# Performance work log

Measured on AMD Instinct MI355X. Metric: run time of the kernel, lower is better.

Reference implementation:

```python
import jax, jax.numpy as jnp
import numpy as np

N_NODES = 100000
N_EDGES = 1_600_000
D_IN = 64
DIM_H = 64


def _film_conv(x, src, dst, W_lin, W_film, b_film, W_skip, W_film_skip):
    """PyG FiLMConv, num_relations=1, aggr='mean', act=ReLU.
    lins/lin_skip have no bias; film has bias; film_skip has no bias."""
    n = x.shape[0]
    # skip/self term: (beta_s, gamma_s) = film_skip(x)
    beta_s, gamma_s = jnp.split(x @ W_film_skip, 2, axis=-1)
    out = jax.nn.relu(gamma_s * (x @ W_skip) + beta_s)
    # relation term: FiLM params from target node i, transform source node j
    beta, gamma = jnp.split(x @ W_film + b_film, 2, axis=-1)  # [N, H] each
    h = x @ W_lin                                             # [N, H]
    msg = jax.nn.relu(gamma[dst] * h[src] + beta[dst])        # [E, H] gather+FiLM
    agg = jax.ops.segment_sum(msg, dst, num_segments=n)       # scatter-sum
    deg = jax.ops.segment_sum(jnp.ones((src.shape[0],), msg.dtype), dst,
                              num_segments=n)
    return out + agg / jnp.maximum(deg, 1.0)[:, None]         # mean aggregation


def setup_inputs() -> dict:
    key = jax.random.key(0)
    ks = jax.random.split(key, 12)
    x = jax.random.normal(ks[0], (N_NODES, D_IN), dtype=jnp.float32)
    edge_index = jax.random.randint(ks[1], (2, N_EDGES), 0, N_NODES, dtype=jnp.int64)
    s_in = 1.0 / np.sqrt(D_IN)
    s_h = 1.0 / np.sqrt(DIM_H)
    params = {
        # layer 1 (D_IN -> DIM_H)
        "W_lin1": jax.random.normal(ks[2], (D_IN, DIM_H), jnp.float32) * s_in,
        "W_film1": jax.random.normal(ks[3], (D_IN, 2 * DIM_H), jnp.float32) * s_in,
        "b_film1": jnp.zeros((2 * DIM_H,), jnp.float32),
        "W_skip1": jax.random.normal(ks[4], (D_IN, DIM_H), jnp.float32) * s_in,
        "W_film_skip1": jax.random.normal(ks[5], (D_IN, 2 * DIM_H), jnp.float32) * s_in,
        # layer 2 (DIM_H -> DIM_H)
        "W_lin2": jax.random.normal(ks[6], (DIM_H, DIM_H), jnp.float32) * s_h,
        "W_film2": jax.random.normal(ks[7], (DIM_H, 2 * DIM_H), jnp.float32) * s_h,
        "b_film2": jnp.zeros((2 * DIM_H,), jnp.float32),
        "W_skip2": jax.random.normal(ks[8], (DIM_H, DIM_H), jnp.float32) * s_h,
        "W_film_skip2": jax.random.normal(ks[9], (DIM_H, 2 * DIM_H), jnp.float32) * s_h,
        # final head
        "W_out": jax.random.normal(ks[10], (DIM_H, 1), jnp.float32) * s_h,
        "b_out": jnp.zeros((1,), jnp.float32),
    }
    return {"x": x, "edge_index": edge_index, **params}


def reference(x, edge_index,
              W_lin1, W_film1, b_film1, W_skip1, W_film_skip1,
              W_lin2, W_film2, b_film2, W_skip2, W_film_skip2,
              W_out, b_out):
    src, dst = edge_index[0], edge_index[1]
    h = _film_conv(x, src, dst, W_lin1, W_film1, b_film1, W_skip1, W_film_skip1)
    h = jax.nn.leaky_relu(h, negative_slope=0.01)
    h = _film_conv(h, src, dst, W_lin2, W_film2, b_film2, W_skip2, W_film_skip2)
    h = jax.nn.leaky_relu(h, negative_slope=0.01)
    return h @ W_out + b_out  # [N, 1]
```

## Files before the change

### kernel.cpp

```cpp
#include <hip/hip_runtime.h>
#include <cstddef>


#define THREADS 256
#define NB 256
#define NPSHIFT 9
#define NPSZ 512

typedef unsigned short u16;
typedef unsigned char u8;
typedef unsigned int u32;
typedef short bf16x8 __attribute__((ext_vector_type(8)));
typedef float f32x4 __attribute__((ext_vector_type(4)));
typedef float f32x2 __attribute__((ext_vector_type(2)));

__device__ __forceinline__ u16 f2b(float f) {
  u32 u = __float_as_uint(f);
  u32 r = (u + 0x7FFFu + ((u >> 16) & 1u)) >> 16;
  return (u16)r;
}
__device__ __forceinline__ float b2f(u16 u) {
  return __uint_as_float(((u32)u) << 16);
}
__device__ __forceinline__ u8 f2fp8(float v) {
  return (u8)(__builtin_amdgcn_cvt_pk_fp8_f32(v, v, 0, false) & 0xFF);
}

struct WSrc {
  const float* p;
  int ld;
  int off;
};
struct WPack {
  WSrc m[12];
};

__global__ __launch_bounds__(THREADS) void prep_and_hist(
    WPack wp, u16* __restrict__ Wp, const int* __restrict__ dst,
    int* __restrict__ counts, int E, int CH, int P) {
  int b = blockIdx.x, t = threadIdx.x;
  if (b < 12) {
    WSrc ws = wp.m[b];
    u16* dstp = Wp + b * 4096;
#pragma unroll
    for (int i = 0; i < 16; ++i) {
      int e = t + 256 * i;
      int n = e >> 6, k = e & 63;
      float v = ws.p[(size_t)k * ws.ld + ws.off + n];
      dstp[e ^ ((n & 7) << 3)] = f2b(v);
    }
    return;
  }
  __shared__ int h[256];
  int hb = b - 12;
  h[t] = 0;
  __syncthreads();
  int lo = hb * CH;
  int hi = min(lo + CH, E);
  for (int i = lo + t; i < hi; i += THREADS) atomicAdd(&h[dst[i] >> NPSHIFT], 1);
  __syncthreads();
  if (t < P) counts[t * NB + hb] = h[t];
}

template <int INBF16>
__global__ __launch_bounds__(THREADS) void gemm_mfma(
    const void* __restrict__ Xv, int N, const u16* __restrict__ WpL,
    const float* __restrict__ bfilm, u8* __restrict__ H8, u16* __restrict__ BETA,
    u16* __restrict__ GAMMA, u16* __restrict__ S) {
  __shared__ u16 XT[64 * 64];
  __shared__ u16 WT[6 * 64 * 64];
  int t = threadIdx.x;
  int row0 = blockIdx.x * 64;

  {
    int row = t >> 2, kq = (t & 3) * 16;
    int gr = row0 + row;
    uint4 w0 = {0, 0, 0, 0}, w1 = {0, 0, 0, 0};
    if (gr < N) {
      if (INBF16) {
        const uint4* xp = (const uint4*)((const u16*)Xv + (size_t)gr * 64 + kq);
        w0 = xp[0];
        w1 = xp[1];
      } else {
        const float* xp = (const float*)Xv + (size_t)gr * 64 + kq;
        float4 f0 = ((const float4*)xp)[0];
        float4 f1 = ((const float4*)xp)[1];
        float4 f2 = ((const float4*)xp)[2];
        float4 f3 = ((const float4*)xp)[3];
        w0.x = f2b(f0.x) | ((u32)f2b(f0.y) << 16);
        w0.y = f2b(f0.z) | ((u32)f2b(f0.w) << 16);
        w0.z = f2b(f1.x) | ((u32)f2b(f1.y) << 16);
        w0.w = f2b(f1.z) | ((u32)f2b(f1.w) << 16);
        w1.x = f2b(f2.x) | ((u32)f2b(f2.y) << 16);
        w1.y = f2b(f2.z) | ((u32)f2b(f2.w) << 16);
        w1.z = f2b(f3.x) | ((u32)f2b(f3.y) << 16);
        w1.w = f2b(f3.z) | ((u32)f2b(f3.w) << 16);
      }
    }
    int e = row * 64 + kq;
    int s = (row & 7) << 3;
    *(uint4*)&XT[e ^ s] = w0;
    *(uint4*)&XT[(e + 8) ^ s] = w1;
  }
  {
    const uint4* wsrc = (const uint4*)WpL;
    uint4* wdst = (uint4*)WT;
    for (int i = t; i < 3072; i += THREADS) wdst[i] = wsrc[i];
  }
  __syncthreads();

  int lane = t & 63, wid = t >> 6;
  int arow = wid * 16 + (lane & 15);
  int kb = (lane >> 4) << 3;
  int as = (arow & 7) << 3;
  bf16x8 A0 = *(const bf16x8*)&XT[(arow * 64 + kb) ^ as];
  bf16x8 A1 = *(const bf16x8*)&XT[(arow * 64 + 32 + kb) ^ as];

  auto bfrag = [&](int mat, int ct, int kk) -> bf16x8 {
    int n = ct * 16 + (lane & 15);
    int e = (n * 64 + kk * 32 + kb) ^ ((n & 7) << 3);
    return *(const bf16x8*)&WT[mat * 4096 + e];
  };

  const f32x4 z = {0.f, 0.f, 0.f, 0.f};
  int rbase = wid * 16 + ((lane >> 4) << 2);
  int cbase = lane & 15;

  {
    f32x4 a0[4], a1[4], a2[4];
#pragma unroll
    for (int ct = 0; ct < 4; ++ct) {
      a0[ct] = z;
      a1[ct] = z;
      a2[ct] = z;
    }
#pragma unroll
    for (int ct = 0; ct < 4; ++ct) {
      a0[ct] = __builtin_amdgcn_mfma_f32_16x16x32_bf16(A0, bfrag(0, ct, 0), a0[ct], 0, 0, 0);
      a0[ct] = __builtin_amdgcn_mfma_f32_16x16x32_bf16(A1, bfrag(0, ct, 1), a0[ct], 0, 0, 0);
      a1[ct] = __builtin_amdgcn_mfma_f32_16x16x32_bf16(A0, bfrag(1, ct, 0), a1[ct], 0, 0, 0);
      a1[ct] = __builtin_amdgcn_mfma_f32_16x16x32_bf16(A1, bfrag(1, ct, 1), a1[ct], 0, 0, 0);
      a2[ct] = __builtin_amdgcn_mfma_f32_16x16x32_bf16(A0, bfrag(2, ct, 0), a2[ct], 0, 0, 0);
      a2[ct] = __builtin_amdgcn_mfma_f32_16x16x32_bf16(A1, bfrag(2, ct, 1), a2[ct], 0, 0, 0);
    }
#pragma unroll
    for (int ct = 0; ct < 4; ++ct) {
      int c = ct * 16 + cbase;
#pragma unroll
      for (int r = 0; r < 4; ++r) {
        int gr = row0 + rbase + r;
        if (gr < N) {
          float v = fmaxf(fmaf(a2[ct][r], a0[ct][r], a1[ct][r]), 0.f);
          S[(size_t)gr * 64 + c] = f2b(v);
        }
      }
    }
  }

  {
    f32x4 a0[4], a1[4], a2[4];
#pragma unroll
    for (int ct = 0; ct < 4; ++ct) {
      a0[ct] = z;
      a1[ct] = z;
      a2[ct] = z;
    }
#pragma unroll
    for (int ct = 0; ct < 4; ++ct) {
      a0[ct] = __builtin_amdgcn_mfma_f32_16x16x32_bf16(A0, bfrag(3, ct, 0), a0[ct], 0, 0, 0);
      a0[ct] = __builtin_amdgcn_mfma_f32_16x16x32_bf16(A1, bfrag(3, ct, 1), a0[ct], 0, 0, 0);
      a1[ct] = __builtin_amdgcn_mfma_f32_16x16x32_bf16(A0, bfrag(4, ct, 0), a1[ct], 0, 0, 0);
      a1[ct] = __builtin_amdgcn_mfma_f32_16x16x32_bf16(A1, bfrag(4, ct, 1), a1[ct], 0, 0, 0);
      a2[ct] = __builtin_amdgcn_mfma_f32_16x16x32_bf16(A0, bfrag(5, ct, 0), a2[ct], 0, 0, 0);
      a2[ct] = __builtin_amdgcn_mfma_f32_16x16x32_bf16(A1, bfrag(5, ct, 1), a2[ct], 0, 0, 0);
    }
#pragma unroll
    for (int ct = 0; ct < 4; ++ct) {
      int c = ct * 16 + cbase;
      float bb = bfilm[c];
      float bg = bfilm[64 + c];
#pragma unroll
      for (int r = 0; r < 4; ++r) {
        int gr = row0 + rbase + r;
        if (gr < N) {
          size_t o = (size_t)gr * 64 + c;
          H8[o] = f2fp8(a0[ct][r]);
          BETA[o] = f2b(a1[ct][r] + bb);
          GAMMA[o] = f2b(a2[ct][r] + bg);
        }
      }
    }
  }
}

__global__ __launch_bounds__(THREADS) void scan_block(int* __restrict__ arr,
                                                      int* __restrict__ bsums, int M) {
  __shared__ int ts[THREADS];
  int t = threadIdx.x;
  int base = blockIdx.x * 1024 + t * 4;
  int v0 = 0, v1 = 0, v2 = 0, v3 = 0;
  if (base + 0 < M) v0 = arr[base + 0];
  if (base + 1 < M) v1 = arr[base + 1];
  if (base + 2 < M) v2 = arr[base + 2];
  if (base + 3 < M) v3 = arr[base + 3];
  int s = v0 + v1 + v2 + v3;
  ts[t] = s;
  __syncthreads();
  for (int off = 1; off < THREADS; off <<= 1) {
    int x = (t >= off) ? ts[t - off] : 0;
    __syncthreads();
    ts[t] += x;
    __syncthreads();
  }
  int eb = ts[t] - s;
  if (base + 0 < M) arr[base + 0] = eb;
  if (base + 1 < M) arr[base + 1] = eb + v0;
  if (base + 2 < M) arr[base + 2] = eb + v0 + v1;
  if (base + 3 < M) arr[base + 3] = eb + v0 + v1 + v2;
  if (t == THREADS - 1) bsums[blockIdx.x] = ts[t];
}

__global__ void scan_tops(int* __restrict__ bsums, int nb) {
  if (threadIdx.x == 0 && blockIdx.x == 0) {
    int run = 0;
    for (int i = 0; i < nb; ++i) {
      int x = bsums[i];
      bsums[i] = run;
      run += x;
    }
  }
}

__global__ __launch_bounds__(THREADS) void scan_fix(int* __restrict__ arr,
                                                    const int* __restrict__ bsums,
                                                    int M, int TOT) {
  int i = blockIdx.x * THREADS + threadIdx.x;
  if (i < M) arr[i] += bsums[i >> 10];
  if (i == 0) arr[M] = TOT;
}

__global__ __launch_bounds__(THREADS) void bucket_scatter(
    const int* __restrict__ src, const int* __restrict__ dst,
    const int* __restrict__ base, u32* __restrict__ buck, int E, int CH, int P) {
  __shared__ int cur[256];
  int b = blockIdx.x, t = threadIdx.x;
  if (t < P) cur[t] = base[t * NB + b];
  __syncthreads();
  int lo = b * CH;
  int hi = min(lo + CH, E);
  for (int i = lo + t; i < hi; i += THREADS) {
    int d = dst[i];
    int pos = atomicAdd(&cur[d >> NPSHIFT], 1);
    buck[pos] = (u32)src[i] | ((u32)(d & (NPSZ - 1)) << 17);
  }
}

__global__ __launch_bounds__(THREADS) void build_csr(
    const u32* __restrict__ buck, const int* __restrict__ base,
    int* __restrict__ rs, int* __restrict__ csr, int* __restrict__ perm,
    int N, int E, int P) {
  __shared__ int hA[NPSZ], hB[NPSZ], cur[NPSZ];
  __shared__ int h64[64], c64[64];
  int p = blockIdx.x, t = threadIdx.x;
  hA[t] = 0;
  hA[t + 256] = 0;
  __syncthreads();
  int pstart = base[p * NB];
  int pend = base[(p + 1) * NB];
  for (int i = pstart + t; i < pend; i += THREADS)
    atomicAdd(&hA[buck[i] >> 17], 1);
  __syncthreads();
  int deg0 = hA[t], deg1 = hA[t + 256];
  int* s = hA;
  int* d2 = hB;
  for (int off = 1; off < NPSZ; off <<= 1) {
#pragma unroll
    for (int r = 0; r < 2; ++r) {
      int idx = t + r * 256;
      int v = s[idx];
      if (idx >= off) v += s[idx - off];
      d2[idx] = v;
    }
    __syncthreads();
    int* tmp = s;
    s = d2;
    d2 = tmp;
  }
#pragma unroll
  for (int r = 0; r < 2; ++r) {
    int idx = t + r * 256;
    int excl = idx ? s[idx - 1] : 0;
    cur[idx] = excl;
    int node = (p << NPSHIFT) + idx;
    if (node < N) rs[node] = pstart + excl;
  }
  if (p == P - 1 && t == 0) rs[N] = E;
  __syncthreads();
  for (int i = pstart + t; i < pend; i += THREADS) {
    u32 w = buck[i];
    int pos = atomicAdd(&cur[w >> 17], 1);
    csr[pstart + pos] = (int)(w & 0x1FFFFu);
  }
  __syncthreads();
  if (t < 64) h64[t] = 0;
  __syncthreads();
  int b0 = min(deg0, 63), b1 = min(deg1, 63);
  atomicAdd(&h64[b0], 1);
  atomicAdd(&h64[b1], 1);
  __syncthreads();
  if (t == 0) {
    int run = 0;
    for (int i = 0; i < 64; ++i) {
      int v = h64[i];
      c64[i] = run;
      run += v;
    }
  }
  __syncthreads();
  int base_out = p << NPSHIFT;
  int pos0 = atomicAdd(&c64[b0], 1);
  perm[base_out + pos0] = base_out + t;
  int pos1 = atomicAdd(&c64[b1], 1);
  perm[base_out + pos1] = base_out + t + 256;
}


template <int FINAL>
__global__ __launch_bounds__(THREADS) void agg_kernel(
    const u8* __restrict__ H8, const u16* __restrict__ GAMMA,
    const u16* __restrict__ BETA, const u16* __restrict__ S,
    const int* __restrict__ rs, const int* __restrict__ csr,
    const int* __restrict__ perm, u16* __restrict__ Xn,
    const float* __restrict__ Wout, const float* __restrict__ bout,
    float* __restrict__ out, int N, int E) {
  int wid = blockIdx.x * 4 + (threadIdx.x >> 6);
  int lane = threadIdx.x & 63;
  int q = lane >> 4;
  int fl = lane & 15;
  int node = perm[wid * 4 + q];
  bool valid = node < N;
  int nd = valid ? node : N - 1;
  int beg = rs[nd];
  int deg = valid ? rs[nd + 1] - beg : 0;
  int m = deg;
  m = max(m, __shfl_xor(m, 16, 64));
  m = max(m, __shfl_xor(m, 32, 64));

  size_t nb4 = (size_t)nd * 16 + fl;
  const uint2* G2 = (const uint2*)GAMMA;
  const uint2* B2 = (const uint2*)BETA;
  const u32* H1 = (const u32*)H8;
  const uint2* S2 = (const uint2*)S;
  uint2 gp = G2[nb4];
  uint2 bp = B2[nb4];

  auto unpA = [](u32 h) -> f32x2 {
    f32x2 r = {__uint_as_float(h << 16), __uint_as_float(h & 0xFFFF0000u)};
    return r;
  };
  f32x2 gA = unpA(gp.x), gB = unpA(gp.y);
  f32x2 bA = unpA(bp.x), bB = unpA(bp.y);
  const f32x2 zz = {0.f, 0.f};
  f32x2 accA = zz, accB = zz;
  int qb = q * 16;

  for (int c = 0; c < m; c += 16) {
    int li = beg + c + fl;
    int idxv = csr[min(li, E - 1)];
    int nin = min(16, m - c);
#pragma unroll 4
    for (int u = 0; u < 16; u += 4) {
      if (u >= nin) break;
      int s0 = __shfl(idxv, qb + u + 0, 64);
      int s1 = __shfl(idxv, qb + u + 1, 64);
      int s2 = __shfl(idxv, qb + u + 2, 64);
      int s3 = __shfl(idxv, qb + u + 3, 64);
      u32 h0 = H1[(size_t)s0 * 16 + fl];
      u32 h1 = H1[(size_t)s1 * 16 + fl];
      u32 h2 = H1[(size_t)s2 * 16 + fl];
      u32 h3 = H1[(size_t)s3 * 16 + fl];
      int e0 = c + u;
      f32x2 lo, hi, mA, mB;
      bool ok;
      lo = __builtin_amdgcn_cvt_pk_f32_fp8((int)h0, false);
      hi = __builtin_amdgcn_cvt_pk_f32_fp8((int)h0, true);
      mA = __builtin_elementwise_max(__builtin_elementwise_fma(gA, lo, bA), zz);
      mB = __builtin_elementwise_max(__builtin_elementwise_fma(gB, hi, bB), zz);
      ok = e0 + 0 < deg;
      accA += ok ? mA : zz;
      accB += ok ? mB : zz;
      lo = __builtin_amdgcn_cvt_pk_f32_fp8((int)h1, false);
      hi = __builtin_amdgcn_cvt_pk_f32_fp8((int)h1, true);
      mA = __builtin_elementwise_max(__builtin_elementwise_fma(gA, lo, bA), zz);
      mB = __builtin_elementwise_max(__builtin_elementwise_fma(gB, hi, bB), zz);
      ok = e0 + 1 < deg;
      accA += ok ? mA : zz;
      accB += ok ? mB : zz;
      lo = __builtin_amdgcn_cvt_pk_f32_fp8((int)h2, false);
      hi = __builtin_amdgcn_cvt_pk_f32_fp8((int)h2, true);
      mA = __builtin_elementwise_max(__builtin_elementwise_fma(gA, lo, bA), zz);
      mB = __builtin_elementwise_max(__builtin_elementwise_fma(gB, hi, bB), zz);
      ok = e0 + 2 < deg;
      accA += ok ? mA : zz;
      accB += ok ? mB : zz;
      lo = __builtin_amdgcn_cvt_pk_f32_fp8((int)h3, false);
      hi = __builtin_amdgcn_cvt_pk_f32_fp8((int)h3, true);
      mA = __builtin_elementwise_max(__builtin_elementwise_fma(gA, lo, bA), zz);
      mB = __builtin_elementwise_max(__builtin_elementwise_fma(gB, hi, bB), zz);
      ok = e0 + 3 < deg;
      accA += ok ? mA : zz;
      accB += ok ? mB : zz;
    }
  }

  float inv = 1.f / fmaxf((float)deg, 1.f);
  uint2 sp = S2[nb4];
  f32x2 sA = unpA(sp.x), sB = unpA(sp.y);
  float v0 = fmaf(accA.x, inv, sA.x);
  float v1 = fmaf(accA.y, inv, sA.y);
  float v2 = fmaf(accB.x, inv, sB.x);
  float v3 = fmaf(accB.y, inv, sB.y);
  v0 = v0 > 0.f ? v0 : 0.01f * v0;
  v1 = v1 > 0.f ? v1 : 0.01f * v1;
  v2 = v2 > 0.f ? v2 : 0.01f * v2;
  v3 = v3 > 0.f ? v3 : 0.01f * v3;
  if (FINAL == 0) {
    if (valid) {
      uint2 pw;
      pw.x = (u32)f2b(v0) | ((u32)f2b(v1) << 16);
      pw.y = (u32)f2b(v2) | ((u32)f2b(v3) << 16);
      ((uint2*)Xn)[nb4] = pw;
    }
  } else {
    float4 w4 = ((const float4*)Wout)[fl];
    float v = fmaf(v0, w4.x, fmaf(v1, w4.y, fmaf(v2, w4.z, v3 * w4.w)));
#pragma unroll
    for (int off = 1; off < 16; off <<= 1) v += __shfl_xor(v, off, 64);
    if (valid && fl == 0) out[node] = v + bout[0];
  }
}

extern "C" void kernel_launch(void* const* d_in, const int* in_sizes, int n_in,
                              void* d_out, int out_size, void* d_ws, size_t ws_size,
                              hipStream_t stream) {
  const float* x = (const float*)d_in[0];
  const int* ei = (const int*)d_in[1];
  const float* Wlin1 = (const float*)d_in[2];
  const float* Wfilm1 = (const float*)d_in[3];
  const float* bfilm1 = (const float*)d_in[4];
  const float* Wskip1 = (const float*)d_in[5];
  const float* Wfs1 = (const float*)d_in[6];
  const float* Wlin2 = (const float*)d_in[7];
  const float* Wfilm2 = (const float*)d_in[8];
  const float* bfilm2 = (const float*)d_in[9];
  const float* Wskip2 = (const float*)d_in[10];
  const float* Wfs2 = (const float*)d_in[11];
  const float* Wout = (const float*)d_in[12];
  const float* bout = (const float*)d_in[13];

  int N = in_sizes[0] / 64;
  int E = in_sizes[1] / 2;
  const int* src = ei;
  const int* dst = ei + E;

  int P = (N + NPSZ - 1) >> NPSHIFT;
  int CH = (E + NB - 1) / NB;
  int M = P * NB;
  int NSLOT = P << NPSHIFT;

  size_t NF = (size_t)N * 64;
  char* p = (char*)d_ws;
  u8* H8 = (u8*)p;
  p += NF * 2;
  u16* BETA = (u16*)p;
  p += NF * 2;
  u16* GAMMA = (u16*)p;
  p += NF * 2;
  u16* S = (u16*)p;
  p += NF * 2;
  u16* X2 = (u16*)p;
  u32* buck = (u32*)p;
  size_t bsz = (size_t)E * 4, xsz = NF * 2;
  p += (bsz > xsz ? bsz : xsz);
  u16* Wp = (u16*)p;
  p += 12 * 4096 * 2;
  int* rs = (int*)p;
  p += (size_t)(N + 2) * 4;
  int* csr = (int*)p;
  p += (size_t)E * 4;
  int* perm = (int*)p;
  p += (size_t)NSLOT * 4;
  int* counts = (int*)p;
  p += (size_t)(M + 2) * 4;
  int* bsums = (int*)p;

  int gemm_blocks = (N + 63) / 64;
  int agg_blocks = NSLOT / 16;
  int nbM = (M + 1023) / 1024;

  WPack wp;
  wp.m[0] = {Wskip1, 64, 0};
  wp.m[1] = {Wfs1, 128, 0};
  wp.m[2] = {Wfs1, 128, 64};
  wp.m[3] = {Wlin1, 64, 0};
  wp.m[4] = {Wfilm1, 128, 0};
  wp.m[5] = {Wfilm1, 128, 64};
  wp.m[6] = {Wskip2, 64, 0};
  wp.m[7] = {Wfs2, 128, 0};
  wp.m[8] = {Wfs2, 128, 64};
  wp.m[9] = {Wlin2, 64, 0};
  wp.m[10] = {Wfilm2, 128, 0};
  wp.m[11] = {Wfilm2, 128, 64};

  prep_and_hist<<<12 + NB, THREADS, 0, stream>>>(wp, Wp, dst, counts, E, CH, P);
  scan_block<<<nbM, THREADS, 0, stream>>>(counts, bsums, M);
  scan_tops<<<1, 64, 0, stream>>>(bsums, nbM);
  scan_fix<<<(M + THREADS - 1) / THREADS, THREADS, 0, stream>>>(counts, bsums, M, E);
  bucket_scatter<<<NB, THREADS, 0, stream>>>(src, dst, counts, buck, E, CH, P);
  build_csr<<<P, THREADS, 0, stream>>>(buck, counts, rs, csr, perm, N, E, P);

  gemm_mfma<0><<<gemm_blocks, THREADS, 0, stream>>>(x, N, Wp, bfilm1, H8, BETA, GAMMA, S);
  agg_kernel<0><<<agg_blocks, THREADS, 0, stream>>>(H8, GAMMA, BETA, S, rs, csr, perm,
                                                    X2, nullptr, nullptr, nullptr, N, E);

  gemm_mfma<1><<<gemm_blocks, THREADS, 0, stream>>>(X2, N, Wp + 6 * 4096, bfilm2, H8,
                                                    BETA, GAMMA, S);
  agg_kernel<1><<<agg_blocks, THREADS, 0, stream>>>(H8, GAMMA, BETA, S, rs, csr, perm,
                                                    nullptr, Wout, bout, (float*)d_out,
                                                    N, E);
}
```

Measured before the change: 198.4 us.

## Replace scan-based bucket offsets with fixed-capacity buckets and atomic cursors

Removes the three-kernel prefix scan over per-block histograms and the separate bucket scatter. Each histogram block reserves space in fixed-capacity per-partition buckets via a global atomic and scatters edges immediately. build_csr then writes per-node begin and degree arrays into padded CSR slots. This cuts several kernel launches and one pass over dst, but assumes no partition exceeds CAP edges and makes edge order within a bucket nondeterministic.

```diff
diff --git a/kernel.cpp b/kernel.cpp
--- a/kernel.cpp
+++ b/kernel.cpp
@@ -6,6 +6,7 @@
 #define NB 256
 #define NPSHIFT 9
 #define NPSZ 512
+#define CAP 10240
 
 typedef unsigned short u16;
 typedef unsigned char u8;
@@ -35,9 +36,10 @@
   WSrc m[12];
 };
 
-__global__ __launch_bounds__(THREADS) void prep_and_hist(
-    WPack wp, u16* __restrict__ Wp, const int* __restrict__ dst,
-    int* __restrict__ counts, int E, int CH, int P) {
+__global__ __launch_bounds__(THREADS) void prep_and_scatter(
+    WPack wp, u16* __restrict__ Wp, const int* __restrict__ src,
+    const int* __restrict__ dst, int* __restrict__ gcur, u32* __restrict__ buck,
+    int E, int CH, int P) {
   int b = blockIdx.x, t = threadIdx.x;
   if (b < 12) {
     WSrc ws = wp.m[b];
@@ -52,6 +54,7 @@
     return;
   }
   __shared__ int h[256];
+  __shared__ int cur[256];
   int hb = b - 12;
   h[t] = 0;
   __syncthreads();
@@ -59,7 +62,16 @@
   int hi = min(lo + CH, E);
   for (int i = lo + t; i < hi; i += THREADS) atomicAdd(&h[dst[i] >> NPSHIFT], 1);
   __syncthreads();
-  if (t < P) counts[t * NB + hb] = h[t];
+  if (t < P) {
+    int base = h[t] ? atomicAdd(&gcur[t], h[t]) : 0;
+    cur[t] = t * CAP + base;
+  }
+  __syncthreads();
+  for (int i = lo + t; i < hi; i += THREADS) {
+    int d = dst[i];
+    int pos = atomicAdd(&cur[d >> NPSHIFT], 1);
+    buck[pos] = (u32)src[i] | ((u32)(d & (NPSZ - 1)) << 17);
+  }
 }
 
 template <int INBF16>
@@ -193,82 +205,19 @@
   }
 }
 
-__global__ __launch_bounds__(THREADS) void scan_block(int* __restrict__ arr,
-                                                      int* __restrict__ bsums, int M) {
-  __shared__ int ts[THREADS];
-  int t = threadIdx.x;
-  int base = blockIdx.x * 1024 + t * 4;
-  int v0 = 0, v1 = 0, v2 = 0, v3 = 0;
-  if (base + 0 < M) v0 = arr[base + 0];
-  if (base + 1 < M) v1 = arr[base + 1];
-  if (base + 2 < M) v2 = arr[base + 2];
-  if (base + 3 < M) v3 = arr[base + 3];
-  int s = v0 + v1 + v2 + v3;
-  ts[t] = s;
-  __syncthreads();
-  for (int off = 1; off < THREADS; off <<= 1) {
-    int x = (t >= off) ? ts[t - off] : 0;
-    __syncthreads();
-    ts[t] += x;
-    __syncthreads();
-  }
-  int eb = ts[t] - s;
-  if (base + 0 < M) arr[base + 0] = eb;
-  if (base + 1 < M) arr[base + 1] = eb + v0;
-  if (base + 2 < M) arr[base + 2] = eb + v0 + v1;
-  if (base + 3 < M) arr[base + 3] = eb + v0 + v1 + v2;
-  if (t == THREADS - 1) bsums[blockIdx.x] = ts[t];
-}
-
-__global__ void scan_tops(int* __restrict__ bsums, int nb) {
-  if (threadIdx.x == 0 && blockIdx.x == 0) {
-    int run = 0;
-    for (int i = 0; i < nb; ++i) {
-      int x = bsums[i];
-      bsums[i] = run;
-      run += x;
-    }
-  }
-}
-
-__global__ __launch_bounds__(THREADS) void scan_fix(int* __restrict__ arr,
-                                                    const int* __restrict__ bsums,
-                                                    int M, int TOT) {
-  int i = blockIdx.x * THREADS + threadIdx.x;
-  if (i < M) arr[i] += bsums[i >> 10];
-  if (i == 0) arr[M] = TOT;
-}
-
-__global__ __launch_bounds__(THREADS) void bucket_scatter(
-    const int* __restrict__ src, const int* __restrict__ dst,
-    const int* __restrict__ base, u32* __restrict__ buck, int E, int CH, int P) {
-  __shared__ int cur[256];
-  int b = blockIdx.x, t = threadIdx.x;
-  if (t < P) cur[t] = base[t * NB + b];
-  __syncthreads();
-  int lo = b * CH;
-  int hi = min(lo + CH, E);
-  for (int i = lo + t; i < hi; i += THREADS) {
-    int d = dst[i];
-    int pos = atomicAdd(&cur[d >> NPSHIFT], 1);
-    buck[pos] = (u32)src[i] | ((u32)(d & (NPSZ - 1)) << 17);
-  }
-}
-
 __global__ __launch_bounds__(THREADS) void build_csr(
-    const u32* __restrict__ buck, const int* __restrict__ base,
-    int* __restrict__ rs, int* __restrict__ csr, int* __restrict__ perm,
-    int N, int E, int P) {
+    const u32* __restrict__ buck, const int* __restrict__ gcur,
+    int* __restrict__ begA, int* __restrict__ degA, int* __restrict__ csr,
+    int* __restrict__ perm, int N, int P) {
   __shared__ int hA[NPSZ], hB[NPSZ], cur[NPSZ];
   __shared__ int h64[64], c64[64];
   int p = blockIdx.x, t = threadIdx.x;
+  int cnt = gcur[p];
+  int pbase = p * CAP;
   hA[t] = 0;
   hA[t + 256] = 0;
   __syncthreads();
-  int pstart = base[p * NB];
-  int pend = base[(p + 1) * NB];
-  for (int i = pstart + t; i < pend; i += THREADS)
-    atomicAdd(&hA[buck[i] >> 17], 1);
+  for (int i = t; i < cnt; i += THREADS) atomicAdd(&hA[buck[pbase + i] >> 17], 1);
   __syncthreads();
   int deg0 = hA[t], deg1 = hA[t + 256];
   int* s = hA;
@@ -292,14 +241,20 @@
     int excl = idx ? s[idx - 1] : 0;
     cur[idx] = excl;
     int node = (p << NPSHIFT) + idx;
-    if (node < N) rs[node] = pstart + excl;
-  }
-  if (p == P - 1 && t == 0) rs[N] = E;
-  __syncthreads();
-  for (int i = pstart + t; i < pend; i += THREADS) {
-    u32 w = buck[i];
+    if (node < N) {
+      begA[node] = pbase + excl;
+      degA[node] = s[idx] - excl;
+    }
+  }
+  __syncthreads();
+  for (int i = t; i < cnt; i += THREADS) {
+    u32 w = buck[pbase + i];
     int pos = atomicAdd(&cur[w >> 17], 1);
-    csr[pstart + pos] = (int)(w & 0x1FFFFu);
+    csr[pbase + pos] = (int)(w & 0x1FFFFu);
+  }
+  {
+    int padend = min(cnt + 160, CAP);
+    for (int i = cnt + t; i < padend; i += THREADS) csr[pbase + i] = 0;
   }
   __syncthreads();
   if (t < 64) h64[t] = 0;
@@ -324,15 +279,14 @@
   perm[base_out + pos1] = base_out + t + 256;
 }
 
-
 template <int FINAL>
 __global__ __launch_bounds__(THREADS) void agg_kernel(
     const u8* __restrict__ H8, const u16* __restrict__ GAMMA,
     const u16* __restrict__ BETA, const u16* __restrict__ S,
-    const int* __restrict__ rs, const int* __restrict__ csr,
-    const int* __restrict__ perm, u16* __restrict__ Xn,
-    const float* __restrict__ Wout, const float* __restrict__ bout,
-    float* __restrict__ out, int N, int E) {
+    const int* __restrict__ begA, const int* __restrict__ degA,
+    const int* __restrict__ csr, const int* __restrict__ perm,
+    u16* __restrict__ Xn, const float* __restrict__ Wout,
+    const float* __restrict__ bout, float* __restrict__ out, int N, int PCAP) {
   int wid = blockIdx.x * 4 + (threadIdx.x >> 6);
   int lane = threadIdx.x & 63;
   int q = lane >> 4;
@@ -340,8 +294,8 @@
   int node = perm[wid * 4 + q];
   bool valid = node < N;
   int nd = valid ? node : N - 1;
-  int beg = rs[nd];
-  int deg = valid ? rs[nd + 1] - beg : 0;
+  int beg = begA[nd];
+  int deg = valid ? degA[nd] : 0;
   int m = deg;
   m = max(m, __shfl_xor(m, 16, 64));
   m = max(m, __shfl_xor(m, 32, 64));
@@ -366,7 +320,7 @@
 
   for (int c = 0; c < m; c += 16) {
     int li = beg + c + fl;
-    int idxv = csr[min(li, E - 1)];
+    int idxv = csr[min(li, PCAP - 1)];
     int nin = min(16, m - c);
 #pragma unroll 4
     for (int u = 0; u < 16; u += 4) {
@@ -465,8 +419,8 @@
 
   int P = (N + NPSZ - 1) >> NPSHIFT;
   int CH = (E + NB - 1) / NB;
-  int M = P * NB;
   int NSLOT = P << NPSHIFT;
+  int PCAP = P * CAP;
 
   size_t NF = (size_t)N * 64;
   char* p = (char*)d_ws;
@@ -480,23 +434,22 @@
   p += NF * 2;
   u16* X2 = (u16*)p;
   u32* buck = (u32*)p;
-  size_t bsz = (size_t)E * 4, xsz = NF * 2;
+  size_t bsz = (size_t)PCAP * 4, xsz = NF * 2;
   p += (bsz > xsz ? bsz : xsz);
   u16* Wp = (u16*)p;
   p += 12 * 4096 * 2;
-  int* rs = (int*)p;
-  p += (size_t)(N + 2) * 4;
+  int* begA = (int*)p;
+  p += (size_t)NSLOT * 4;
+  int* degA = (int*)p;
+  p += (size_t)NSLOT * 4;
   int* csr = (int*)p;
-  p += (size_t)E * 4;
+  p += (size_t)PCAP * 4;
   int* perm = (int*)p;
   p += (size_t)NSLOT * 4;
-  int* counts = (int*)p;
-  p += (size_t)(M + 2) * 4;
-  int* bsums = (int*)p;
+  int* gcur = (int*)p;
 
   int gemm_blocks = (N + 63) / 64;
   int agg_blocks = NSLOT / 16;
-  int nbM = (M + 1023) / 1024;
 
   WPack wp;
   wp.m[0] = {Wskip1, 64, 0};
@@ -512,20 +465,19 @@
   wp.m[10] = {Wfilm2, 128, 0};
   wp.m[11] = {Wfilm2, 128, 64};
 
-  prep_and_hist<<<12 + NB, THREADS, 0, stream>>>(wp, Wp, dst, counts, E, CH, P);
-  scan_block<<<nbM, THREADS, 0, stream>>>(counts, bsums, M);
-  scan_tops<<<1, 64, 0, stream>>>(bsums, nbM);
-  scan_fix<<<(M + THREADS - 1) / THREADS, THREADS, 0, stream>>>(counts, bsums, M, E);
-  bucket_scatter<<<NB, THREADS, 0, stream>>>(src, dst, counts, buck, E, CH, P);
-  build_csr<<<P, THREADS, 0, stream>>>(buck, counts, rs, csr, perm, N, E, P);
+  hipMemsetAsync(gcur, 0, 256 * sizeof(int), stream);
+  prep_and_scatter<<<12 + NB, THREADS, 0, stream>>>(wp, Wp, src, dst, gcur, buck, E,
+                                                    CH, P);
+  build_csr<<<P, THREADS, 0, stream>>>(buck, gcur, begA, degA, csr, perm, N, P);
 
   gemm_mfma<0><<<gemm_blocks, THREADS, 0, stream>>>(x, N, Wp, bfilm1, H8, BETA, GAMMA, S);
-  agg_kernel<0><<<agg_blocks, THREADS, 0, stream>>>(H8, GAMMA, BETA, S, rs, csr, perm,
-                                                    X2, nullptr, nullptr, nullptr, N, E);
+  agg_kernel<0><<<agg_blocks, THREADS, 0, stream>>>(H8, GAMMA, BETA, S, begA, degA, csr,
+                                                    perm, X2, nullptr, nullptr, nullptr,
+                                                    N, PCAP);
 
   gemm_mfma<1><<<gemm_blocks, THREADS, 0, stream>>>(X2, N, Wp + 6 * 4096, bfilm2, H8,
                                                     BETA, GAMMA, S);
-  agg_kernel<1><<<agg_blocks, THREADS, 0, stream>>>(H8, GAMMA, BETA, S, rs, csr, perm,
-                                                    nullptr, Wout, bout, (float*)d_out,
-                                                    N, E);
-}
+  agg_kernel<1><<<agg_blocks, THREADS, 0, stream>>>(H8, GAMMA, BETA, S, begA, degA, csr,
+                                                    perm, nullptr, Wout, bout,
+                                                    (float*)d_out, N, PCAP);
+}
```

New measurement: 191.3 us. -3.6%, faster.
